# Performance work log

Measured on AMD Instinct MI355X. Metric: run time of the kernel, lower is better.

Reference implementation:

```python
import jax, jax.numpy as jnp
import numpy as np

B, S, H, C = 2, 128, 768, 5
NEG = -1024.0

def setup_inputs() -> dict:
    key = jax.random.key(0)
    ks = jax.random.split(key, 6)
    sequence_output = jax.random.normal(ks[0], (B, S, H), dtype=jnp.float32)
    attention_mask = jnp.ones((B, S), dtype=jnp.int32)
    ng_token_mask = jax.random.bernoulli(ks[1], 0.5, (B, S, C, S))  # bool
    target = (jax.random.uniform(ks[2], (B, S, C, S)) < 0.01).astype(jnp.float32)
    lim = 1.0 / np.sqrt(H)
    W_prd = jax.random.uniform(ks[3], (H, H), jnp.float32, -lim, lim)
    b_prd = jnp.zeros((H,), jnp.float32)
    W_arg = jax.random.uniform(ks[4], (C * H, H), jnp.float32, -lim, lim)
    b_arg = jnp.zeros((C * H,), jnp.float32)
    W_out = jax.random.uniform(ks[5], (C, H), jnp.float32, -lim, lim)
    return dict(sequence_output=sequence_output, attention_mask=attention_mask,
                ng_token_mask=ng_token_mask, target=target,
                W_prd=W_prd, b_prd=b_prd, W_arg=W_arg, b_arg=b_arg, W_out=W_out)

def reference(sequence_output, attention_mask, ng_token_mask, target,
              W_prd, b_prd, W_arg, b_arg, W_out):
    b, s, h = sequence_output.shape
    c = W_out.shape[0]
    # get_mask: ng mask restricted to attended tokens, then any over case dim
    mask = ng_token_mask & (attention_mask[:, None, None, :] > 0)   # (B,S,C,S)
    mask = jnp.any(mask, axis=2, keepdims=True)                      # (B,S,1,S)
    # dropout is identity in eval mode
    h_p = sequence_output @ W_prd.T + b_prd                          # (B,S,H)
    h_a = (sequence_output @ W_arg.T + b_arg).reshape(b, s, c, h)    # (B,S,C,H)
    # outer-sum biaffine: (B, S_prd, S_arg, C, H)
    hh = jnp.tanh(h_p[:, :, None, None, :] + h_a[:, None, :, :, :])
    # per-case Linear(H,1,bias=False), stacked at dim=2 -> (B, S_prd, C, S_arg)
    output = jnp.einsum('bpach,ch->bpca', hh, W_out)
    output = output + (~mask).astype(output.dtype) * NEG
    # cross_entropy_pas_loss: multi-hot CE over candidate (last) axis
    log_sm = jax.nn.log_softmax(output, axis=3)
    loss = jnp.sum(-log_sm * target) / jnp.sum(target)
    return loss, output
```

## Files before the change

### kernel.cpp

```cpp
#include <hip/hip_runtime.h>
#include <math.h>

#define Bb 2
#define Ss 128
#define Hh 768
#define Cc 5
#define Mm 256
#define NEGV -1024.0f
#define SCALE 2.8853900817779268f

#define PT 2
#define NBLK (Mm / PT * Cc)

typedef __attribute__((ext_vector_type(8))) short bf16x8;
typedef __attribute__((ext_vector_type(4))) float f32x4;
typedef unsigned short ushort;

__device__ __forceinline__ unsigned pack_hi16(float hi, float lo) {
    return (__float_as_uint(hi) & 0xFFFF0000u) | (__float_as_uint(lo) >> 16);
}
__device__ __forceinline__ bf16x8 pack_bf16x8(float4 lo, float4 hi) {
    union { bf16x8 v; unsigned u[4]; } r;
    r.u[0] = pack_hi16(lo.y, lo.x);
    r.u[1] = pack_hi16(lo.w, lo.z);
    r.u[2] = pack_hi16(hi.y, hi.x);
    r.u[3] = pack_hi16(hi.w, hi.z);
    return r.v;
}
__device__ __forceinline__ ushort bf16_rne(float f) {
    unsigned b = __float_as_uint(f);
    return (ushort)((b + 0x7FFFu + ((b >> 16) & 1u)) >> 16);
}

#define SB __builtin_amdgcn_sched_barrier(0);


__global__ __launch_bounds__(256)
void gemm_mfma(const float* __restrict__ X,
               const float* __restrict__ Wprd,
               const float* __restrict__ Warg,
               const float* __restrict__ bprd,
               const float* __restrict__ barg,
               float* __restrict__ EpG,
               ushort* __restrict__ haTb,
               float* __restrict__ accum)
{
    __shared__ __align__(16) ushort Asb[64][72];
    __shared__ __align__(16) ushort Bsb[32][72];

    if (blockIdx.x == 0 && blockIdx.y == 0 && threadIdx.x == 0) {
        accum[0] = 0.f; accum[1] = 0.f;
        ((unsigned*)accum)[2] = 0u;
    }
    const int bm   = blockIdx.x;
    const int bn   = blockIdx.y;
    const int tid  = threadIdx.x;
    const int wave = tid >> 6;
    const int lane = tid & 63;
    const int l16  = lane & 15;
    const int quad = lane >> 4;

    const float* Wsrc; const float* bsrc;
    const int nb = bn * 32;
    if (nb < Hh) { Wsrc = Wprd + (size_t)nb * Hh;        bsrc = bprd + nb; }
    else         { Wsrc = Warg + (size_t)(nb - Hh) * Hh; bsrc = barg + (nb - Hh); }

    const int srow = tid >> 2;
    const int sko  = (tid & 3) * 8;
    const float* gA = X + (size_t)(bm * 64 + srow) * Hh + sko;
    const float* gB = Wsrc + (size_t)(tid >> 2) * Hh + sko;

    float4 a00 = *(const float4*)(gA);
    float4 a01 = *(const float4*)(gA + 4);
    float4 a10 = *(const float4*)(gA + 32);
    float4 a11 = *(const float4*)(gA + 36);
    float4 b00, b01, b10, b11;
    if (tid < 128) {
        b00 = *(const float4*)(gB);      b01 = *(const float4*)(gB + 4);
        b10 = *(const float4*)(gB + 32); b11 = *(const float4*)(gB + 36);
    }

    f32x4 acc0 = {0.f,0.f,0.f,0.f}, acc1 = {0.f,0.f,0.f,0.f};

    for (int k0 = 0; k0 < Hh; k0 += 64) {
        *(bf16x8*)&Asb[srow][sko]      = pack_bf16x8(a00, a01);
        *(bf16x8*)&Asb[srow][sko + 32] = pack_bf16x8(a10, a11);
        if (tid < 128) {
            *(bf16x8*)&Bsb[tid >> 2][sko]      = pack_bf16x8(b00, b01);
            *(bf16x8*)&Bsb[tid >> 2][sko + 32] = pack_bf16x8(b10, b11);
        }
        __syncthreads();
        if (k0 + 64 < Hh) {
            a00 = *(const float4*)(gA + k0 + 64);
            a01 = *(const float4*)(gA + k0 + 68);
            a10 = *(const float4*)(gA + k0 + 96);
            a11 = *(const float4*)(gA + k0 + 100);
            if (tid < 128) {
                b00 = *(const float4*)(gB + k0 + 64);
                b01 = *(const float4*)(gB + k0 + 68);
                b10 = *(const float4*)(gB + k0 + 96);
                b11 = *(const float4*)(gB + k0 + 100);
            }
        }
        {
            bf16x8 af0 = *(const bf16x8*)&Asb[wave * 16 + l16][quad * 8];
            bf16x8 c00 = *(const bf16x8*)&Bsb[l16][quad * 8];
            bf16x8 c10 = *(const bf16x8*)&Bsb[16 + l16][quad * 8];
            acc0 = __builtin_amdgcn_mfma_f32_16x16x32_bf16(af0, c00, acc0, 0, 0, 0);
            acc1 = __builtin_amdgcn_mfma_f32_16x16x32_bf16(af0, c10, acc1, 0, 0, 0);
            bf16x8 af1 = *(const bf16x8*)&Asb[wave * 16 + l16][quad * 8 + 32];
            bf16x8 c01 = *(const bf16x8*)&Bsb[l16][quad * 8 + 32];
            bf16x8 c11 = *(const bf16x8*)&Bsb[16 + l16][quad * 8 + 32];
            acc0 = __builtin_amdgcn_mfma_f32_16x16x32_bf16(af1, c01, acc0, 0, 0, 0);
            acc1 = __builtin_amdgcn_mfma_f32_16x16x32_bf16(af1, c11, acc1, 0, 0, 0);
        }
        __syncthreads();
    }

    const float sb0 = SCALE * bsrc[l16];
    const float sb1 = SCALE * bsrc[16 + l16];
    const int row = bm * 64 + wave * 16 + quad * 4;

    if (nb < Hh) {
        #pragma unroll
        for (int r = 0; r < 4; ++r) {
            const int mm = row + r;
            EpG[(size_t)mm * Hh + nb + l16]      = __builtin_amdgcn_exp2f(SCALE * acc0[r] + sb0);
            EpG[(size_t)mm * Hh + nb + 16 + l16] = __builtin_amdgcn_exp2f(SCALE * acc1[r] + sb1);
        }
    } else {
        const int q  = nb - Hh;
        const int cU = q / Hh;
        const int h0 = q % Hh;
        const int hA = h0 + l16;
        const int hB = h0 + 16 + l16;
        const size_t offA = (size_t)(hA >> 3) * 1024 + (hA & 7);
        const size_t offB = (size_t)(hB >> 3) * 1024 + (hB & 7);
        #pragma unroll
        for (int r = 0; r < 4; ++r) {
            const int mm = row + r;
            const int bI = mm >> 7, aI = mm & 127;
            const size_t base = ((size_t)(bI * Cc + cU) * 96) * 1024 + (size_t)aI * 8;
            const float e0 = __builtin_amdgcn_exp2f(SCALE * acc0[r] + sb0);
            const float e1 = __builtin_amdgcn_exp2f(SCALE * acc1[r] + sb1);
            haTb[base + offA] = bf16_rne(e0);
            haTb[base + offB] = bf16_rne(e1);
        }
    }
}

#define LOADG4(R, g) \
    R##0 = hap4[((g)*4+0)*128]; R##1 = hap4[((g)*4+1)*128]; \
    R##2 = hap4[((g)*4+2)*128]; R##3 = hap4[((g)*4+3)*128];

#define PAIR(z, ee) { \
    const float ww = wS[hx + (z)]; \
    const float r0 = __builtin_amdgcn_rcpf(fmaf(e0S[hx + (z)], (ee), 1.0f)); \
    const float r1 = __builtin_amdgcn_rcpf(fmaf(e1S[hx + (z)], (ee), 1.0f)); \
    if ((z) & 1) { ac01 = fmaf(ww, r0, ac01); ac11 = fmaf(ww, r1, ac11); } \
    else         { ac00 = fmaf(ww, r0, ac00); ac10 = fmaf(ww, r1, ac10); } \
}

#define C1(u, hx_) { \
    const int hx = (hx_); \
    PAIR(0, __uint_as_float((u).x << 16)) \
    PAIR(1, __uint_as_float((u).x & 0xFFFF0000u)) \
    PAIR(2, __uint_as_float((u).y << 16)) \
    PAIR(3, __uint_as_float((u).y & 0xFFFF0000u)) \
    PAIR(4, __uint_as_float((u).z << 16)) \
    PAIR(5, __uint_as_float((u).z & 0xFFFF0000u)) \
    PAIR(6, __uint_as_float((u).w << 16)) \
    PAIR(7, __uint_as_float((u).w & 0xFFFF0000u)) \
}

#define CONSUMEG4(R, g) \
    C1(R##0, hbase + ((g)*4+0)*8)  C1(R##1, hbase + ((g)*4+1)*8) \
    C1(R##2, hbase + ((g)*4+2)*8)  C1(R##3, hbase + ((g)*4+3)*8)

__global__ __launch_bounds__(512, 4)
void biaffine_loss(const float* __restrict__ EpG,
                   const ushort* __restrict__ haTb,
                   const float* __restrict__ Wout,
                   const int* __restrict__ ng,
                   const int* __restrict__ att,
                   const float* __restrict__ target,
                   float* __restrict__ out_logits,
                   float* __restrict__ accum,
                   float* __restrict__ out_loss)
{
    __shared__ float partial[PT][3][Ss];
    __shared__ float maskneg[PT][Ss];
    __shared__ float redmax[PT][2];
    __shared__ float red3[PT][2][3];
    __shared__ float swr_s;
    __shared__ __align__(16) float wS[Hh];
    __shared__ __align__(16) float e0S[Hh];
    __shared__ __align__(16) float e1S[Hh];

    const int L   = ((int)blockIdx.x & 7) * 80 + ((int)blockIdx.x >> 3);
    const int g   = L >> 6;
    const int j   = L & 63;
    const int b   = (g >= Cc) ? 1 : 0;
    const int c   = g - b * Cc;
    const int bp0 = (b * 64 + j) * PT;
    const int tid = threadIdx.x;
    const int a   = tid & (Ss - 1);
    const int hq  = __builtin_amdgcn_readfirstlane(tid >> 7);
    const int lane = tid & 63;

    const float* wrow = Wout + (size_t)c * Hh;
    const float* ep0  = EpG + (size_t)(bp0 + 0) * Hh;
    const float* ep1  = EpG + (size_t)(bp0 + 1) * Hh;

    if (tid < PT * Ss) {
        const int p_i = tid >> 7;
        const int aa  = tid & (Ss - 1);
        const int attv = att[b * Ss + aa];
        const int* ngp = ng + (size_t)(bp0 + p_i) * Cc * Ss + aa;
        const int n0 = ngp[0 * Ss], n1 = ngp[1 * Ss], n2 = ngp[2 * Ss],
                  n3 = ngp[3 * Ss], n4 = ngp[4 * Ss];
        const int any = (n0 | n1 | n2 | n3 | n4) & (attv > 0 ? -1 : 0);
        maskneg[p_i][aa] = any ? 0.0f : NEGV;
    }

    if (tid < 64) {
        float s = 0.f;
        #pragma unroll
        for (int i = 0; i < Hh / 64; ++i) s += wrow[tid + i * 64];
        #pragma unroll
        for (int off = 32; off; off >>= 1) s += __shfl_xor(s, off, 64);
        if (tid == 0) swr_s = s;
    }

    for (int i = tid; i < Hh; i += 512) {
        wS[i]  = wrow[i];
        e0S[i] = ep0[i];
        e1S[i] = ep1[i];
    }

    const uint4* hap4 = (const uint4*)(haTb + ((size_t)(b * Cc + c) * 96) * 1024)
                      + (size_t)hq * 24 * 128 + a;
    const int hbase = hq * 192;

    uint4 A0, A1, A2, A3;
    uint4 B0, B1, B2, B3;
    float ac00 = 0.f, ac01 = 0.f, ac10 = 0.f, ac11 = 0.f;

    LOADG4(A, 0)
    LOADG4(B, 1)
    __syncthreads();
    CONSUMEG4(A, 0)  LOADG4(A, 2)  SB
    CONSUMEG4(B, 1)  LOADG4(B, 3)  SB
    CONSUMEG4(A, 2)  LOADG4(A, 4)  SB
    CONSUMEG4(B, 3)  LOADG4(B, 5)  SB
    CONSUMEG4(A, 4)
    CONSUMEG4(B, 5)

    if (hq != 0) {
        partial[0][hq - 1][a] = ac00 + ac01;
        partial[1][hq - 1][a] = ac10 + ac11;
    }
    __syncthreads();

    float logit[PT];
    const int wv = tid >> 6;
    if (hq == 0) {
        const float ps[PT] = { ac00 + ac01, ac10 + ac11 };
        #pragma unroll
        for (int p = 0; p < PT; ++p) {
            const float full = ps[p] + partial[p][0][a] + partial[p][1][a] + partial[p][2][a];
            logit[p] = swr_s - 2.0f * full + maskneg[p][a];
            out_logits[((size_t)(bp0 + p) * Cc + c) * Ss + a] = logit[p];
            float mx = logit[p];
            #pragma unroll
            for (int off = 32; off; off >>= 1) mx = fmaxf(mx, __shfl_xor(mx, off, 64));
            if (lane == 0) redmax[p][wv] = mx;
        }
    }
    __syncthreads();

    if (hq == 0) {
        #pragma unroll
        for (int p = 0; p < PT; ++p) {
            const float rm = fmaxf(redmax[p][0], redmax[p][1]);
            const float e  = __builtin_amdgcn_exp2f((logit[p] - rm) * 1.4426950408889634f);
            const float tg = target[((size_t)(bp0 + p) * Cc + c) * Ss + a];
            float se = e, st = tg, sx = tg * logit[p];
            #pragma unroll
            for (int off = 32; off; off >>= 1) {
                se += __shfl_xor(se, off, 64);
                st += __shfl_xor(st, off, 64);
                sx += __shfl_xor(sx, off, 64);
            }
            if (lane == 0) { red3[p][wv][0] = se; red3[p][wv][1] = st; red3[p][wv][2] = sx; }
        }
    }
    __syncthreads();

    if (tid == 0) {
        float nsum = 0.f, dsum = 0.f;
        #pragma unroll
        for (int p = 0; p < PT; ++p) {
            const float rm = fmaxf(redmax[p][0], redmax[p][1]);
            const float SE = red3[p][0][0] + red3[p][1][0];
            const float ST = red3[p][0][1] + red3[p][1][1];
            const float SX = red3[p][0][2] + red3[p][1][2];
            const float lse = rm + __builtin_amdgcn_logf(SE) * 0.6931471805599453f;
            nsum += lse * ST - SX;
            dsum += ST;
        }
        atomicAdd(&accum[0], nsum);
        atomicAdd(&accum[1], dsum);
        __threadfence();
        const unsigned old = atomicAdd((unsigned*)(accum + 2), 1u);
        if (old == (unsigned)(NBLK - 1)) {
            const float n = atomicAdd(&accum[0], 0.0f);
            const float d = atomicAdd(&accum[1], 0.0f);
            out_loss[0] = n / d;
        }
    }
}

extern "C" void kernel_launch(void* const* d_in, const int* in_sizes, int n_in,
                              void* d_out, int out_size, void* d_ws, size_t ws_size,
                              hipStream_t stream) {
    const float* seq    = (const float*)d_in[0];
    const int*   att    = (const int*)  d_in[1];
    const int*   ng     = (const int*)  d_in[2];
    const float* target = (const float*)d_in[3];
    const float* Wprd   = (const float*)d_in[4];
    const float* bprd   = (const float*)d_in[5];
    const float* Warg   = (const float*)d_in[6];
    const float* barg   = (const float*)d_in[7];
    const float* Wout   = (const float*)d_in[8];

    float*  out    = (float*)d_out;
    float*  EpG    = (float*)d_ws;
    ushort* haTb   = (ushort*)(EpG + 196608);
    float*  accum  = EpG + 196608 + 491520;

    gemm_mfma<<<dim3(4, 144), 256, 0, stream>>>(seq, Wprd, Warg, bprd, barg,
                                                EpG, haTb, accum);
    biaffine_loss<<<dim3(NBLK), 512, 0, stream>>>(EpG, haTb, Wout, ng, att, target,
                                                  out + 1, accum, out);
}
```

Measured before the change: 128.3 us.

## Split hidden dim across eight waves with two arg-columns per lane in biaffine kernel

Each wave in the biaffine loss kernel now covers a 96-wide slice of the hidden dimension for all 128 arg positions, with each lane handling two arg columns, instead of four 128-thread groups each covering 192 hidden units. The wOut and e_p values are read from LDS as float4 and reused across both columns, which cuts LDS traffic per rcp. The final softmax/loss reduction is folded into a single wave, removing two block barriers and the shared redmax/red3 staging. In exchange there is a larger 7-way partial-sum reduction in LDS and more accumulator registers per thread.

```diff
diff --git a/kernel.cpp b/kernel.cpp
--- a/kernel.cpp
+++ b/kernel.cpp
@@ -33,7 +33,6 @@
 }
 
 #define SB __builtin_amdgcn_sched_barrier(0);
-
 
 __global__ __launch_bounds__(256)
 void gemm_mfma(const float* __restrict__ X,
@@ -149,33 +148,40 @@
     }
 }
 
+
 #define LOADG4(R, g) \
-    R##0 = hap4[((g)*4+0)*128]; R##1 = hap4[((g)*4+1)*128]; \
-    R##2 = hap4[((g)*4+2)*128]; R##3 = hap4[((g)*4+3)*128];
-
-#define PAIR(z, ee) { \
-    const float ww = wS[hx + (z)]; \
-    const float r0 = __builtin_amdgcn_rcpf(fmaf(e0S[hx + (z)], (ee), 1.0f)); \
-    const float r1 = __builtin_amdgcn_rcpf(fmaf(e1S[hx + (z)], (ee), 1.0f)); \
-    if ((z) & 1) { ac01 = fmaf(ww, r0, ac01); ac11 = fmaf(ww, r1, ac11); } \
-    else         { ac00 = fmaf(ww, r0, ac00); ac10 = fmaf(ww, r1, ac10); } \
-}
-
-#define C1(u, hx_) { \
+    R##0 = hap4[(g)*256];       R##1 = hap4[(g)*256 + 64]; \
+    R##2 = hap4[(g)*256 + 128]; R##3 = hap4[(g)*256 + 192];
+
+#define TERM(ww, q0, q1, ea0, ea1, A00, A01, A10, A11) { \
+    float r; \
+    r = __builtin_amdgcn_rcpf(fmaf((q0), (ea0), 1.0f)); A00 = fmaf((ww), r, A00); \
+    r = __builtin_amdgcn_rcpf(fmaf((q1), (ea0), 1.0f)); A10 = fmaf((ww), r, A10); \
+    r = __builtin_amdgcn_rcpf(fmaf((q0), (ea1), 1.0f)); A01 = fmaf((ww), r, A01); \
+    r = __builtin_amdgcn_rcpf(fmaf((q1), (ea1), 1.0f)); A11 = fmaf((ww), r, A11); \
+}
+
+#define C2(uA, uB, hx_) { \
     const int hx = (hx_); \
-    PAIR(0, __uint_as_float((u).x << 16)) \
-    PAIR(1, __uint_as_float((u).x & 0xFFFF0000u)) \
-    PAIR(2, __uint_as_float((u).y << 16)) \
-    PAIR(3, __uint_as_float((u).y & 0xFFFF0000u)) \
-    PAIR(4, __uint_as_float((u).z << 16)) \
-    PAIR(5, __uint_as_float((u).z & 0xFFFF0000u)) \
-    PAIR(6, __uint_as_float((u).w << 16)) \
-    PAIR(7, __uint_as_float((u).w & 0xFFFF0000u)) \
-}
-
-#define CONSUMEG4(R, g) \
-    C1(R##0, hbase + ((g)*4+0)*8)  C1(R##1, hbase + ((g)*4+1)*8) \
-    C1(R##2, hbase + ((g)*4+2)*8)  C1(R##3, hbase + ((g)*4+3)*8)
+    const float4 w4a = *(const float4*)&wS[hx];      \
+    const float4 w4b = *(const float4*)&wS[hx + 4];  \
+    const float4 q04a = *(const float4*)&e0S[hx];    \
+    const float4 q04b = *(const float4*)&e0S[hx + 4];\
+    const float4 q14a = *(const float4*)&e1S[hx];    \
+    const float4 q14b = *(const float4*)&e1S[hx + 4];\
+    TERM(w4a.x, q04a.x, q14a.x, __uint_as_float((uA).x << 16),         __uint_as_float((uB).x << 16),         acE00, acE01, acE10, acE11) \
+    TERM(w4a.y, q04a.y, q14a.y, __uint_as_float((uA).x & 0xFFFF0000u), __uint_as_float((uB).x & 0xFFFF0000u), acO00, acO01, acO10, acO11) \
+    TERM(w4a.z, q04a.z, q14a.z, __uint_as_float((uA).y << 16),         __uint_as_float((uB).y << 16),         acE00, acE01, acE10, acE11) \
+    TERM(w4a.w, q04a.w, q14a.w, __uint_as_float((uA).y & 0xFFFF0000u), __uint_as_float((uB).y & 0xFFFF0000u), acO00, acO01, acO10, acO11) \
+    TERM(w4b.x, q04b.x, q14b.x, __uint_as_float((uA).z << 16),         __uint_as_float((uB).z << 16),         acE00, acE01, acE10, acE11) \
+    TERM(w4b.y, q04b.y, q14b.y, __uint_as_float((uA).z & 0xFFFF0000u), __uint_as_float((uB).z & 0xFFFF0000u), acO00, acO01, acO10, acO11) \
+    TERM(w4b.z, q04b.z, q14b.z, __uint_as_float((uA).w << 16),         __uint_as_float((uB).w << 16),         acE00, acE01, acE10, acE11) \
+    TERM(w4b.w, q04b.w, q14b.w, __uint_as_float((uA).w & 0xFFFF0000u), __uint_as_float((uB).w & 0xFFFF0000u), acO00, acO01, acO10, acO11) \
+}
+
+#define CONSUMEG(R, g) \
+    C2(R##0, R##1, hq96 + ((g)*2 + 0) * 8) \
+    C2(R##2, R##3, hq96 + ((g)*2 + 1) * 8)
 
 __global__ __launch_bounds__(512, 4)
 void biaffine_loss(const float* __restrict__ EpG,
@@ -188,10 +194,8 @@
                    float* __restrict__ accum,
                    float* __restrict__ out_loss)
 {
-    __shared__ float partial[PT][3][Ss];
+    __shared__ float partial[PT][7][Ss];
     __shared__ float maskneg[PT][Ss];
-    __shared__ float redmax[PT][2];
-    __shared__ float red3[PT][2][3];
     __shared__ float swr_s;
     __shared__ __align__(16) float wS[Hh];
     __shared__ __align__(16) float e0S[Hh];
@@ -203,10 +207,10 @@
     const int b   = (g >= Cc) ? 1 : 0;
     const int c   = g - b * Cc;
     const int bp0 = (b * 64 + j) * PT;
-    const int tid = threadIdx.x;
-    const int a   = tid & (Ss - 1);
-    const int hq  = __builtin_amdgcn_readfirstlane(tid >> 7);
+    const int tid  = threadIdx.x;
     const int lane = tid & 63;
+    const int wvid = __builtin_amdgcn_readfirstlane(tid >> 6);
+    const int hq96 = wvid * 96;
 
     const float* wrow = Wout + (size_t)c * Hh;
     const float* ep0  = EpG + (size_t)(bp0 + 0) * Hh;
@@ -239,84 +243,77 @@
     }
 
     const uint4* hap4 = (const uint4*)(haTb + ((size_t)(b * Cc + c) * 96) * 1024)
-                      + (size_t)hq * 24 * 128 + a;
-    const int hbase = hq * 192;
+                      + (size_t)wvid * 12 * 128 + lane;
 
     uint4 A0, A1, A2, A3;
     uint4 B0, B1, B2, B3;
-    float ac00 = 0.f, ac01 = 0.f, ac10 = 0.f, ac11 = 0.f;
+    float acE00 = 0.f, acO00 = 0.f;
+    float acE01 = 0.f, acO01 = 0.f;
+    float acE10 = 0.f, acO10 = 0.f;
+    float acE11 = 0.f, acO11 = 0.f;
 
     LOADG4(A, 0)
     LOADG4(B, 1)
     __syncthreads();
-    CONSUMEG4(A, 0)  LOADG4(A, 2)  SB
-    CONSUMEG4(B, 1)  LOADG4(B, 3)  SB
-    CONSUMEG4(A, 2)  LOADG4(A, 4)  SB
-    CONSUMEG4(B, 3)  LOADG4(B, 5)  SB
-    CONSUMEG4(A, 4)
-    CONSUMEG4(B, 5)
-
-    if (hq != 0) {
-        partial[0][hq - 1][a] = ac00 + ac01;
-        partial[1][hq - 1][a] = ac10 + ac11;
+    CONSUMEG(A, 0)  LOADG4(A, 2)  SB
+    CONSUMEG(B, 1)  LOADG4(B, 3)  SB
+    CONSUMEG(A, 2)  LOADG4(A, 4)  SB
+    CONSUMEG(B, 3)  LOADG4(B, 5)  SB
+    CONSUMEG(A, 4)
+    CONSUMEG(B, 5)
+
+    if (wvid != 0) {
+        partial[0][wvid - 1][lane]      = acE00 + acO00;
+        partial[0][wvid - 1][lane + 64] = acE01 + acO01;
+        partial[1][wvid - 1][lane]      = acE10 + acO10;
+        partial[1][wvid - 1][lane + 64] = acE11 + acO11;
     }
     __syncthreads();
 
-    float logit[PT];
-    const int wv = tid >> 6;
-    if (hq == 0) {
-        const float ps[PT] = { ac00 + ac01, ac10 + ac11 };
+    if (wvid == 0) {
+        float nsum = 0.f, dsum = 0.f;
         #pragma unroll
         for (int p = 0; p < PT; ++p) {
-            const float full = ps[p] + partial[p][0][a] + partial[p][1][a] + partial[p][2][a];
-            logit[p] = swr_s - 2.0f * full + maskneg[p][a];
-            out_logits[((size_t)(bp0 + p) * Cc + c) * Ss + a] = logit[p];
-            float mx = logit[p];
+            float f0 = (p == 0) ? (acE00 + acO00) : (acE10 + acO10);
+            float f1 = (p == 0) ? (acE01 + acO01) : (acE11 + acO11);
+            #pragma unroll
+            for (int k = 0; k < 7; ++k) {
+                f0 += partial[p][k][lane];
+                f1 += partial[p][k][lane + 64];
+            }
+            const float l0 = swr_s - 2.0f * f0 + maskneg[p][lane];
+            const float l1 = swr_s - 2.0f * f1 + maskneg[p][lane + 64];
+            const size_t obase = ((size_t)(bp0 + p) * Cc + c) * Ss;
+            out_logits[obase + lane]      = l0;
+            out_logits[obase + lane + 64] = l1;
+            float mx = fmaxf(l0, l1);
             #pragma unroll
             for (int off = 32; off; off >>= 1) mx = fmaxf(mx, __shfl_xor(mx, off, 64));
-            if (lane == 0) redmax[p][wv] = mx;
-        }
-    }
-    __syncthreads();
-
-    if (hq == 0) {
-        #pragma unroll
-        for (int p = 0; p < PT; ++p) {
-            const float rm = fmaxf(redmax[p][0], redmax[p][1]);
-            const float e  = __builtin_amdgcn_exp2f((logit[p] - rm) * 1.4426950408889634f);
-            const float tg = target[((size_t)(bp0 + p) * Cc + c) * Ss + a];
-            float se = e, st = tg, sx = tg * logit[p];
+            const float e = __builtin_amdgcn_exp2f((l0 - mx) * 1.4426950408889634f)
+                          + __builtin_amdgcn_exp2f((l1 - mx) * 1.4426950408889634f);
+            const float tg0 = target[obase + lane];
+            const float tg1 = target[obase + lane + 64];
+            float se = e, st = tg0 + tg1, sx = tg0 * l0 + tg1 * l1;
             #pragma unroll
             for (int off = 32; off; off >>= 1) {
                 se += __shfl_xor(se, off, 64);
                 st += __shfl_xor(st, off, 64);
                 sx += __shfl_xor(sx, off, 64);
             }
-            if (lane == 0) { red3[p][wv][0] = se; red3[p][wv][1] = st; red3[p][wv][2] = sx; }
-        }
-    }
-    __syncthreads();
-
-    if (tid == 0) {
-        float nsum = 0.f, dsum = 0.f;
-        #pragma unroll
-        for (int p = 0; p < PT; ++p) {
-            const float rm = fmaxf(redmax[p][0], redmax[p][1]);
-            const float SE = red3[p][0][0] + red3[p][1][0];
-            const float ST = red3[p][0][1] + red3[p][1][1];
-            const float SX = red3[p][0][2] + red3[p][1][2];
-            const float lse = rm + __builtin_amdgcn_logf(SE) * 0.6931471805599453f;
-            nsum += lse * ST - SX;
-            dsum += ST;
-        }
-        atomicAdd(&accum[0], nsum);
-        atomicAdd(&accum[1], dsum);
-        __threadfence();
-        const unsigned old = atomicAdd((unsigned*)(accum + 2), 1u);
-        if (old == (unsigned)(NBLK - 1)) {
-            const float n = atomicAdd(&accum[0], 0.0f);
-            const float d = atomicAdd(&accum[1], 0.0f);
-            out_loss[0] = n / d;
+            const float lse = mx + __builtin_amdgcn_logf(se) * 0.6931471805599453f;
+            nsum += lse * st - sx;
+            dsum += st;
+        }
+        if (lane == 0) {
+            atomicAdd(&accum[0], nsum);
+            atomicAdd(&accum[1], dsum);
+            __threadfence();
+            const unsigned old = atomicAdd((unsigned*)(accum + 2), 1u);
+            if (old == (unsigned)(NBLK - 1)) {
+                const float n = atomicAdd(&accum[0], 0.0f);
+                const float d = atomicAdd(&accum[1], 0.0f);
+                out_loss[0] = n / d;
+            }
         }
     }
 }
```

Result: no change. 128.0 us (-0.2%).
